# Performance work log

Hardware: AMD Instinct MI355X
Metric: run time of the kernel (lower is better)

## Reference

```python
import jax, jax.numpy as jnp
import numpy as np

H = 2048      # hidden_size
NH = 16       # num_heads
HD = H // NH  # head_dim
B, T = 2, 2048


def setup_inputs() -> dict:
    key = jax.random.key(0)
    ks = jax.random.split(key, 5)
    s = 1.0 / np.sqrt(H)
    return {
        "x": jax.random.normal(ks[0], (B, T, H), dtype=jnp.float32),
        "wq": jax.random.normal(ks[1], (H, H), dtype=jnp.float32) * s,
        "bq": jnp.zeros((H,), dtype=jnp.float32),
        "wk": jax.random.normal(ks[2], (H, H), dtype=jnp.float32) * s,
        "bk": jnp.zeros((H,), dtype=jnp.float32),
        "wv": jax.random.normal(ks[3], (H, H), dtype=jnp.float32) * s,
        "bv": jnp.zeros((H,), dtype=jnp.float32),
        "wo": jax.random.normal(ks[4], (H, H), dtype=jnp.float32) * s,
        "bo": jnp.zeros((H,), dtype=jnp.float32),
    }


def reference(x, wq, bq, wk, bk, wv, bv, wo, bo):
    Bx, Tx, C = x.shape
    # projections (torch Linear: x @ W.T + b)
    q = x @ wq.T + bq
    k = x @ wk.T + bk
    v = x @ wv.T + bv
    # [B, T, H] -> [B, NH, T, HD]
    q = q.reshape(Bx, Tx, NH, HD).transpose(0, 2, 1, 3)
    k = k.reshape(Bx, Tx, NH, HD).transpose(0, 2, 1, 3)
    v = v.reshape(Bx, Tx, NH, HD).transpose(0, 2, 1, 3)
    scale = 1.0 / np.sqrt(HD).astype(np.float32)
    scores = jnp.einsum('bhqd,bhkd->bhqk', q, k) * scale  # [B, NH, T, T]
    causal = jnp.tril(jnp.ones((Tx, Tx), dtype=bool))
    scores = jnp.where(causal[None, None], scores, -jnp.inf)
    attn = jax.nn.softmax(scores, axis=-1)
    out = jnp.einsum('bhqk,bhkd->bhqd', attn, v)  # [B, NH, T, HD]
    out = out.transpose(0, 2, 1, 3).reshape(Bx, Tx, C)
    return out @ wo.T + bo
```

## Files before the change

### kernel.cpp

```cpp
#include <hip/hip_runtime.h>
#include <stdint.h>

constexpr int H_  = 2048;
constexpr int NH_ = 16;
constexpr int HD_ = 128;
constexpr int B_  = 2;
constexpr int T_  = 2048;
constexpr int M_  = B_ * T_;

typedef unsigned short u16;
typedef __bf16 bf16x8 __attribute__((ext_vector_type(8)));
typedef float  f32x4  __attribute__((ext_vector_type(4)));

__device__ __forceinline__ u16 f2bf(float f) {
  uint32_t u = __builtin_bit_cast(uint32_t, f);
  u += 0x7fffu + ((u >> 16) & 1u);
  return (u16)(u >> 16);
}

__device__ __forceinline__ void gload_lds16(const void* g, void* lds) {
  auto gp = (const __attribute__((address_space(1))) uint32_t*)(uintptr_t)g;
  auto lp = (__attribute__((address_space(3))) uint32_t*)(uint32_t)(uintptr_t)lds;
  __builtin_amdgcn_global_load_lds(gp, lp, 16, 0, 0);
}

__device__ __forceinline__ f32x4 mfma16(bf16x8 a, bf16x8 b, f32x4 c) {
  return __builtin_amdgcn_mfma_f32_16x16x32_bf16(a, b, c, 0, 0, 0);
}

__global__ __launch_bounds__(256) void cvt_kernel(const float* __restrict__ s,
                                                  u16* __restrict__ d, int n4) {
  int i = blockIdx.x * 256 + threadIdx.x;
  if (i < n4) {
    float4 v = ((const float4*)s)[i];
    ushort4 o;
    o.x = f2bf(v.x); o.y = f2bf(v.y); o.z = f2bf(v.z); o.w = f2bf(v.w);
    ((ushort4*)d)[i] = o;
  }
}

template <int OUTF32>
__global__ __launch_bounds__(256) void gemm_bt(const u16* __restrict__ A,
                                               const u16* __restrict__ Bm,
                                               const float* __restrict__ bias,
                                               void* __restrict__ Cout,
                                               int M, int N, int K) {
  __shared__ u16 As[2][128 * 64];
  __shared__ u16 Bs[2][128 * 64];
  const int tid = threadIdx.x;
  const int wave = tid >> 6, lane = tid & 63, l15 = lane & 15, lhi = lane >> 4;
  const int tm = blockIdx.x % (M >> 7), tn = blockIdx.x / (M >> 7);
  const int m0 = tm << 7, n0 = tn << 7;
  const int wr = wave >> 1, wc = wave & 1;
  const int NT = K >> 6;

  f32x4 acc[4][4] = {};

  auto stage = [&](int kt, int buf) {
#pragma unroll
    for (int is = 0; is < 4; ++is) {
      int o  = is * 4096 + tid * 16;
      int row = o >> 7;
      int sw  = o ^ (((o >> 7) & 7) << 4);
      int c8  = (sw >> 4) & 7;
      gload_lds16(A + (size_t)(m0 + row) * K + kt * 64 + c8 * 8,
                  &As[buf][0] + (is * 2048 + wave * 512));
      gload_lds16(Bm + (size_t)(n0 + row) * K + kt * 64 + c8 * 8,
                  &Bs[buf][0] + (is * 2048 + wave * 512));
    }
  };

  stage(0, 0);
  __syncthreads();
  int cur = 0;
  for (int kt = 0; kt < NT; ++kt) {
    if (kt + 1 < NT) stage(kt + 1, cur ^ 1);
#pragma unroll
    for (int kk = 0; kk < 2; ++kk) {
      bf16x8 af[4], bfr[4];
#pragma unroll
      for (int mi = 0; mi < 4; ++mi) {
        int row = wr * 64 + mi * 16 + l15;
        int ob  = (row * 128 + kk * 64 + lhi * 16) ^ ((row & 7) << 4);
        af[mi] = *(const bf16x8*)((const char*)&As[cur][0] + ob);
      }
#pragma unroll
      for (int ni = 0; ni < 4; ++ni) {
        int row = wc * 64 + ni * 16 + l15;
        int ob  = (row * 128 + kk * 64 + lhi * 16) ^ ((row & 7) << 4);
        bfr[ni] = *(const bf16x8*)((const char*)&Bs[cur][0] + ob);
      }
#pragma unroll
      for (int mi = 0; mi < 4; ++mi)
#pragma unroll
        for (int ni = 0; ni < 4; ++ni)
          acc[mi][ni] = mfma16(af[mi], bfr[ni], acc[mi][ni]);
    }
    __syncthreads();
    cur ^= 1;
  }

  float bv[4];
#pragma unroll
  for (int ni = 0; ni < 4; ++ni) bv[ni] = bias[n0 + wc * 64 + ni * 16 + l15];
#pragma unroll
  for (int mi = 0; mi < 4; ++mi) {
#pragma unroll
    for (int ni = 0; ni < 4; ++ni) {
      int n = n0 + wc * 64 + ni * 16 + l15;
#pragma unroll
      for (int r = 0; r < 4; ++r) {
        int m = m0 + wr * 64 + mi * 16 + lhi * 4 + r;
        float v = acc[mi][ni][r] + bv[ni];
        if (OUTF32)
          ((float*)Cout)[(size_t)m * N + n] = v;
        else
          ((u16*)Cout)[(size_t)m * N + n] = f2bf(v);
      }
    }
  }
}

__global__ __launch_bounds__(256) void transpose_v(const u16* __restrict__ V,
                                                   u16* __restrict__ Vt) {
  __shared__ u16 tile[32][33];
  int bh = blockIdx.z, b = bh >> 4, h = bh & 15;
  int t0 = blockIdx.x * 32, d0 = blockIdx.y * 32;
  int x = threadIdx.x, y = threadIdx.y;
#pragma unroll
  for (int k = 0; k < 4; ++k) {
    int t = y + k * 8;
    tile[t][x] = V[(size_t)(b * T_ + t0 + t) * H_ + h * HD_ + d0 + x];
  }
  __syncthreads();
#pragma unroll
  for (int k = 0; k < 4; ++k) {
    int d = y + k * 8;
    Vt[((size_t)(bh * HD_ + d0 + d)) * T_ + t0 + x] = tile[x][d];
  }
}

__global__ __launch_bounds__(256) void attn_kernel(const u16* __restrict__ Q,
                                                   const u16* __restrict__ K,
                                                   const u16* __restrict__ Vt,
                                                   u16* __restrict__ ctx) {
  __shared__ u16 Ks[2][64 * 128];
  __shared__ u16 Vs[2][128 * 64];
  __shared__ u16 Ps[4][1024];

  const int tid = threadIdx.x, wave = tid >> 6, lane = tid & 63;
  const int l15 = lane & 15, lhi = lane >> 4;
  const int bh = blockIdx.y, b = bh >> 4, h = bh & 15;
  const int nQB = T_ / 64;
  const int qbs[2] = {(int)blockIdx.x, nQB - 1 - (int)blockIdx.x};

  const float C1  = 0.08838834764831845f * 1.4426950408889634f;
  const float THR = 11.5f;

  auto stage = [&](int buf, int kv0) {
#pragma unroll
    for (int is = 0; is < 4; ++is) {
      {
        int o_ = is * 4096 + tid * 16;
        int row = o_ >> 8;
        int sw = o_ ^ (((o_ >> 8) & 7) << 4);
        int c8 = (sw >> 4) & 15;
        gload_lds16(K + (size_t)(b * T_ + kv0 + row) * H_ + h * HD_ + c8 * 8,
                    &Ks[buf][0] + (is * 2048 + wave * 512));
      }
      {
        int o_ = is * 4096 + tid * 16;
        int row = o_ >> 7;
        int sw = o_ ^ (((o_ >> 7) & 7) << 4);
        int t8 = (sw >> 4) & 7;
        gload_lds16(Vt + (size_t)(bh * HD_ + row) * T_ + kv0 + t8 * 8,
                    &Vs[buf][0] + (is * 2048 + wave * 512));
      }
    }
  };

  stage(0, 0);
  __syncthreads();
  int cur = 0;

  for (int s = 0; s < 2; ++s) {
    const int qb = qbs[s];
    const int q0 = qb * 64 + wave * 16;

    bf16x8 qf[4];
    const u16* qbase = Q + (size_t)(b * T_ + q0 + l15) * H_ + h * HD_ + lhi * 8;
#pragma unroll
    for (int kk = 0; kk < 4; ++kk) qf[kk] = *(const bf16x8*)(qbase + kk * 32);

    f32x4 o[8] = {};
    float m2[4], lr[4];
#pragma unroll
    for (int r = 0; r < 4; ++r) { m2[r] = -__builtin_inff(); lr[r] = 0.f; }

    for (int kvb = 0; kvb <= qb; ++kvb) {
      const int kv0 = kvb * 64;

      const bool has_next = (kvb < qb) || (s == 0);
      if (has_next) stage(cur ^ 1, (kvb < qb) ? (kvb + 1) * 64 : 0);

      f32x4 sv[4];
#pragma unroll
      for (int kt = 0; kt < 4; ++kt) {
        f32x4 sacc = {0.f, 0.f, 0.f, 0.f};
#pragma unroll
        for (int kk = 0; kk < 4; ++kk) {
          int row = kt * 16 + l15;
          int ob = (row * 256 + kk * 64 + lhi * 16) ^ ((row & 7) << 4);
          bf16x8 kf = *(const bf16x8*)((const char*)&Ks[cur][0] + ob);
          sacc = mfma16(qf[kk], kf, sacc);
        }
        sv[kt] = sacc;
      }

      float pmax2[4];
#pragma unroll
      for (int r = 0; r < 4; ++r) pmax2[r] = -__builtin_inff();
      if (kvb == qb) {
#pragma unroll
        for (int kt = 0; kt < 4; ++kt) {
          int key = kv0 + kt * 16 + l15;
#pragma unroll
          for (int r = 0; r < 4; ++r) {
            int q = q0 + lhi * 4 + r;
            float z = sv[kt][r] * C1;
            z = (key <= q) ? z : -__builtin_inff();
            sv[kt][r] = z;
            pmax2[r] = fmaxf(pmax2[r], z);
          }
        }
      } else {
#pragma unroll
        for (int kt = 0; kt < 4; ++kt)
#pragma unroll
          for (int r = 0; r < 4; ++r) {
            float z = sv[kt][r] * C1;
            sv[kt][r] = z;
            pmax2[r] = fmaxf(pmax2[r], z);
          }
      }
#pragma unroll
      for (int r = 0; r < 4; ++r)
#pragma unroll
        for (int d = 1; d < 16; d <<= 1)
          pmax2[r] = fmaxf(pmax2[r], __shfl_xor(pmax2[r], d));

      bool need = false;
#pragma unroll
      for (int r = 0; r < 4; ++r) need |= (pmax2[r] - m2[r] > THR);
      if (__any(need)) {
#pragma unroll
        for (int r = 0; r < 4; ++r) {
          float mn = fmaxf(m2[r], pmax2[r]);
          float al = exp2f(m2[r] - mn);
          m2[r] = mn;
          lr[r] *= al;
#pragma unroll
          for (int dt = 0; dt < 8; ++dt) o[dt][r] *= al;
        }
      }

      float rs[4] = {0.f, 0.f, 0.f, 0.f};
#pragma unroll
      for (int kt = 0; kt < 4; ++kt)
#pragma unroll
        for (int r = 0; r < 4; ++r) {
          float p = exp2f(sv[kt][r] - m2[r]);
          sv[kt][r] = p;
          rs[r] += p;
        }
#pragma unroll
      for (int r = 0; r < 4; ++r) {
#pragma unroll
        for (int d = 1; d < 16; d <<= 1) rs[r] += __shfl_xor(rs[r], d);
        lr[r] += rs[r];
      }

#pragma unroll
      for (int kt = 0; kt < 4; ++kt) {
        int keyl = kt * 16 + l15;
        int slot = keyl >> 3;
#pragma unroll
        for (int r = 0; r < 4; ++r)
          Ps[wave][slot * 128 + (lhi * 4 + r) * 8 + (keyl & 7)] =
              f2bf(sv[kt][r]);
      }
      asm volatile("" ::: "memory");

#pragma unroll
      for (int ks = 0; ks < 2; ++ks) {
        bf16x8 pf = *(const bf16x8*)&Ps[wave][(ks * 4 + lhi) * 128 + l15 * 8];
#pragma unroll
        for (int dt = 0; dt < 8; ++dt) {
          int row = dt * 16 + l15;
          int ob = (row * 128 + ks * 64 + lhi * 16) ^ ((row & 7) << 4);
          bf16x8 vf = *(const bf16x8*)((const char*)&Vs[cur][0] + ob);
          o[dt] = mfma16(pf, vf, o[dt]);
        }
      }
      __syncthreads();
      cur ^= 1;
    }

    float inv[4];
#pragma unroll
    for (int r = 0; r < 4; ++r) inv[r] = 1.0f / lr[r];
#pragma unroll
    for (int dt = 0; dt < 8; ++dt)
#pragma unroll
      for (int r = 0; r < 4; ++r) {
        float v = o[dt][r] * inv[r];
        ctx[(size_t)(b * T_ + q0 + lhi * 4 + r) * H_ + h * HD_ + dt * 16 +
            l15] = f2bf(v);
      }
  }
}

extern "C" void kernel_launch(void* const* d_in, const int* in_sizes, int n_in,
                              void* d_out, int out_size, void* d_ws,
                              size_t ws_size, hipStream_t stream) {
  const float* x  = (const float*)d_in[0];
  const float* wq = (const float*)d_in[1];
  const float* bq = (const float*)d_in[2];
  const float* wk = (const float*)d_in[3];
  const float* bk = (const float*)d_in[4];
  const float* wv = (const float*)d_in[5];
  const float* bv = (const float*)d_in[6];
  const float* wo = (const float*)d_in[7];
  const float* bo = (const float*)d_in[8];

  char* ws = (char*)d_ws;
  constexpr size_t SZ_X = (size_t)M_ * H_ * 2;
  constexpr size_t SZ_W = (size_t)H_ * H_ * 2;
  u16* xb  = (u16*)(ws);
  u16* wqb = (u16*)(ws + SZ_X);
  u16* wkb = (u16*)(ws + SZ_X + 1 * SZ_W);
  u16* wvb = (u16*)(ws + SZ_X + 2 * SZ_W);
  u16* wob = (u16*)(ws + SZ_X + 3 * SZ_W);
  u16* Qb  = (u16*)(ws + 1 * SZ_X + 4 * SZ_W);
  u16* Kb  = (u16*)(ws + 2 * SZ_X + 4 * SZ_W);
  u16* Vb  = (u16*)(ws + 3 * SZ_X + 4 * SZ_W);
  u16* Vtb = (u16*)(ws + 4 * SZ_X + 4 * SZ_W);
  u16* ctx = xb;

  cvt_kernel<<<(M_ * H_) / 1024, 256, 0, stream>>>(x, xb, (M_ * H_) / 4);
  cvt_kernel<<<(H_ * H_) / 1024, 256, 0, stream>>>(wq, wqb, (H_ * H_) / 4);
  cvt_kernel<<<(H_ * H_) / 1024, 256, 0, stream>>>(wk, wkb, (H_ * H_) / 4);
  cvt_kernel<<<(H_ * H_) / 1024, 256, 0, stream>>>(wv, wvb, (H_ * H_) / 4);
  cvt_kernel<<<(H_ * H_) / 1024, 256, 0, stream>>>(wo, wob, (H_ * H_) / 4);

  gemm_bt<0><<<512, 256, 0, stream>>>(xb, wqb, bq, Qb, M_, H_, H_);
  gemm_bt<0><<<512, 256, 0, stream>>>(xb, wkb, bk, Kb, M_, H_, H_);
  gemm_bt<0><<<512, 256, 0, stream>>>(xb, wvb, bv, Vb, M_, H_, H_);

  transpose_v<<<dim3(T_ / 32, HD_ / 32, B_ * NH_), dim3(32, 8), 0, stream>>>(
      Vb, Vtb);

  attn_kernel<<<dim3(T_ / 128, B_ * NH_), 256, 0, stream>>>(Qb, Kb, Vtb, ctx);

  gemm_bt<1><<<512, 256, 0, stream>>>(ctx, wob, bo, d_out, M_, H_, H_);
}
```

Measured before the change: 278.3 us.

## Restructure attention loop: swapped QK MFMA, XCD-aware grid, split waitcnt barriers

The attention kernel now computes S transposed (K as the A operand), so each lane owns one query row and the max/sum reductions need two cross-row shuffles instead of four rows of 4-step shuffles. P is written as packed ushort4 into a swizzled LDS layout to cut bank conflicts. The full __syncthreads is replaced by explicit vmcnt waits plus s_barrier, so the next KV tile's loads can stay in flight, and s_setprio raises wave priority around the MFMA sections. The grid becomes 1D with an XCD-aware mapping that keeps the blocks of each head on the same XCD for L2 reuse. The code relies on hand-placed waitcnt values that depend on how many loads each stage issues.

Result: faster. 256.9 us (-7.7%).

```diff
diff --git a/kernel.cpp b/kernel.cpp
--- a/kernel.cpp
+++ b/kernel.cpp
@@ -150,12 +150,18 @@
 
   const int tid = threadIdx.x, wave = tid >> 6, lane = tid & 63;
   const int l15 = lane & 15, lhi = lane >> 4;
-  const int bh = blockIdx.y, b = bh >> 4, h = bh & 15;
+
+  const int bid = blockIdx.x;
+  const int xcd = bid & 7, idx = bid >> 3;
+  const int bh = xcd * 4 + (idx & 3);
+  const int qi = idx >> 2;
+  const int b = bh >> 4, h = bh & 15;
   const int nQB = T_ / 64;
-  const int qbs[2] = {(int)blockIdx.x, nQB - 1 - (int)blockIdx.x};
+  const int qbs[2] = {qi, nQB - 1 - qi};
 
   const float C1  = 0.08838834764831845f * 1.4426950408889634f;
   const float THR = 11.5f;
+  const float NI  = -__builtin_inff();
 
   auto stage = [&](int buf, int kv0) {
 #pragma unroll
@@ -180,12 +186,15 @@
   };
 
   stage(0, 0);
-  __syncthreads();
+  asm volatile("s_waitcnt vmcnt(0)" ::: "memory");
+  __builtin_amdgcn_s_barrier();
+  asm volatile("" ::: "memory");
   int cur = 0;
 
   for (int s = 0; s < 2; ++s) {
     const int qb = qbs[s];
     const int q0 = qb * 64 + wave * 16;
+    const int qrow = q0 + l15;
 
     bf16x8 qf[4];
     const u16* qbase = Q + (size_t)(b * T_ + q0 + l15) * H_ + h * HD_ + lhi * 8;
@@ -193,17 +202,22 @@
     for (int kk = 0; kk < 4; ++kk) qf[kk] = *(const bf16x8*)(qbase + kk * 32);
 
     f32x4 o[8] = {};
-    float m2[4], lr[4];
-#pragma unroll
-    for (int r = 0; r < 4; ++r) { m2[r] = -__builtin_inff(); lr[r] = 0.f; }
+    float m2 = NI, lr = 0.f;
 
     for (int kvb = 0; kvb <= qb; ++kvb) {
       const int kv0 = kvb * 64;
-
       const bool has_next = (kvb < qb) || (s == 0);
-      if (has_next) stage(cur ^ 1, (kvb < qb) ? (kvb + 1) * 64 : 0);
+      if (has_next) {
+        stage(cur ^ 1, (kvb < qb) ? kv0 + 64 : 0);
+        asm volatile("s_waitcnt vmcnt(8)" ::: "memory");
+      } else {
+        asm volatile("s_waitcnt vmcnt(0)" ::: "memory");
+      }
+      __builtin_amdgcn_s_barrier();
+      asm volatile("" ::: "memory");
 
       f32x4 sv[4];
+      __builtin_amdgcn_s_setprio(1);
 #pragma unroll
       for (int kt = 0; kt < 4; ++kt) {
         f32x4 sacc = {0.f, 0.f, 0.f, 0.f};
@@ -212,27 +226,24 @@
           int row = kt * 16 + l15;
           int ob = (row * 256 + kk * 64 + lhi * 16) ^ ((row & 7) << 4);
           bf16x8 kf = *(const bf16x8*)((const char*)&Ks[cur][0] + ob);
-          sacc = mfma16(qf[kk], kf, sacc);
+          sacc = mfma16(kf, qf[kk], sacc);
         }
         sv[kt] = sacc;
       }
-
-      float pmax2[4];
-#pragma unroll
-      for (int r = 0; r < 4; ++r) pmax2[r] = -__builtin_inff();
+      __builtin_amdgcn_s_setprio(0);
+
+      float pmax2 = NI;
       if (kvb == qb) {
 #pragma unroll
-        for (int kt = 0; kt < 4; ++kt) {
-          int key = kv0 + kt * 16 + l15;
+        for (int kt = 0; kt < 4; ++kt)
 #pragma unroll
           for (int r = 0; r < 4; ++r) {
-            int q = q0 + lhi * 4 + r;
+            int key = kv0 + kt * 16 + lhi * 4 + r;
             float z = sv[kt][r] * C1;
-            z = (key <= q) ? z : -__builtin_inff();
+            z = (key <= qrow) ? z : NI;
             sv[kt][r] = z;
-            pmax2[r] = fmaxf(pmax2[r], z);
+            pmax2 = fmaxf(pmax2, z);
           }
-        }
       } else {
 #pragma unroll
         for (int kt = 0; kt < 4; ++kt)
@@ -240,60 +251,58 @@
           for (int r = 0; r < 4; ++r) {
             float z = sv[kt][r] * C1;
             sv[kt][r] = z;
-            pmax2[r] = fmaxf(pmax2[r], z);
+            pmax2 = fmaxf(pmax2, z);
           }
       }
-#pragma unroll
-      for (int r = 0; r < 4; ++r)
-#pragma unroll
-        for (int d = 1; d < 16; d <<= 1)
-          pmax2[r] = fmaxf(pmax2[r], __shfl_xor(pmax2[r], d));
-
-      bool need = false;
-#pragma unroll
-      for (int r = 0; r < 4; ++r) need |= (pmax2[r] - m2[r] > THR);
-      if (__any(need)) {
+      pmax2 = fmaxf(pmax2, __shfl_xor(pmax2, 16));
+      pmax2 = fmaxf(pmax2, __shfl_xor(pmax2, 32));
+
+      if (__any(pmax2 - m2 > THR)) {
+        float mn = fmaxf(m2, pmax2);
+        float al = exp2f(m2 - mn);
+        m2 = mn;
+        lr *= al;
+        float alo[4];
+#pragma unroll
+        for (int r = 0; r < 4; ++r) alo[r] = __shfl(al, lhi * 4 + r);
+#pragma unroll
+        for (int dt = 0; dt < 8; ++dt)
+#pragma unroll
+          for (int r = 0; r < 4; ++r) o[dt][r] *= alo[r];
+      }
+
+      float rs = 0.f;
+#pragma unroll
+      for (int kt = 0; kt < 4; ++kt)
 #pragma unroll
         for (int r = 0; r < 4; ++r) {
-          float mn = fmaxf(m2[r], pmax2[r]);
-          float al = exp2f(m2[r] - mn);
-          m2[r] = mn;
-          lr[r] *= al;
-#pragma unroll
-          for (int dt = 0; dt < 8; ++dt) o[dt][r] *= al;
+          float p = exp2f(sv[kt][r] - m2);
+          sv[kt][r] = p;
+          rs += p;
         }
-      }
-
-      float rs[4] = {0.f, 0.f, 0.f, 0.f};
-#pragma unroll
-      for (int kt = 0; kt < 4; ++kt)
-#pragma unroll
-        for (int r = 0; r < 4; ++r) {
-          float p = exp2f(sv[kt][r] - m2[r]);
-          sv[kt][r] = p;
-          rs[r] += p;
-        }
-#pragma unroll
-      for (int r = 0; r < 4; ++r) {
-#pragma unroll
-        for (int d = 1; d < 16; d <<= 1) rs[r] += __shfl_xor(rs[r], d);
-        lr[r] += rs[r];
-      }
+      rs += __shfl_xor(rs, 16);
+      rs += __shfl_xor(rs, 32);
+      lr += rs;
 
 #pragma unroll
       for (int kt = 0; kt < 4; ++kt) {
-        int keyl = kt * 16 + l15;
-        int slot = keyl >> 3;
-#pragma unroll
-        for (int r = 0; r < 4; ++r)
-          Ps[wave][slot * 128 + (lhi * 4 + r) * 8 + (keyl & 7)] =
-              f2bf(sv[kt][r]);
+        int slot = kt * 2 + (lhi >> 1);
+        ushort4 pk;
+        pk.x = f2bf(sv[kt][0]);
+        pk.y = f2bf(sv[kt][1]);
+        pk.z = f2bf(sv[kt][2]);
+        pk.w = f2bf(sv[kt][3]);
+        *(ushort4*)&Ps[wave][slot * 128 + ((l15 * 8) ^ ((slot & 7) << 3)) +
+                             (lhi & 1) * 4] = pk;
       }
       asm volatile("" ::: "memory");
 
+      __builtin_amdgcn_s_setprio(1);
 #pragma unroll
       for (int ks = 0; ks < 2; ++ks) {
-        bf16x8 pf = *(const bf16x8*)&Ps[wave][(ks * 4 + lhi) * 128 + l15 * 8];
+        int slot = ks * 4 + lhi;
+        bf16x8 pf = *(const bf16x8*)&Ps[wave][slot * 128 +
+                                              ((l15 * 8) ^ ((slot & 7) << 3))];
 #pragma unroll
         for (int dt = 0; dt < 8; ++dt) {
           int row = dt * 16 + l15;
@@ -302,18 +311,24 @@
           o[dt] = mfma16(pf, vf, o[dt]);
         }
       }
-      __syncthreads();
+      __builtin_amdgcn_s_setprio(0);
+
+      __builtin_amdgcn_s_barrier();
+      asm volatile("" ::: "memory");
       cur ^= 1;
     }
 
-    float inv[4];
-#pragma unroll
-    for (int r = 0; r < 4; ++r) inv[r] = 1.0f / lr[r];
+    float invo[4];
+    {
+      float inv = 1.0f / lr;
+#pragma unroll
+      for (int r = 0; r < 4; ++r) invo[r] = __shfl(inv, lhi * 4 + r);
+    }
 #pragma unroll
     for (int dt = 0; dt < 8; ++dt)
 #pragma unroll
       for (int r = 0; r < 4; ++r) {
-        float v = o[dt][r] * inv[r];
+        float v = o[dt][r] * invo[r];
         ctx[(size_t)(b * T_ + q0 + lhi * 4 + r) * H_ + h * HD_ + dt * 16 +
             l15] = f2bf(v);
       }
@@ -360,7 +375,7 @@
   transpose_v<<<dim3(T_ / 32, HD_ / 32, B_ * NH_), dim3(32, 8), 0, stream>>>(
       Vb, Vtb);
 
-  attn_kernel<<<dim3(T_ / 128, B_ * NH_), 256, 0, stream>>>(Qb, Kb, Vtb, ctx);
+  attn_kernel<<<512, 256, 0, stream>>>(Qb, Kb, Vtb, ctx);
 
   gemm_bt<1><<<512, 256, 0, stream>>>(ctx, wob, bo, d_out, M_, H_, H_);
 }
```
